# Optimization experiments

Measured on AMD Instinct MI355X. Metric: run time of the kernel, lower is better.

The kernel has to match this reference:

```python
import jax, jax.numpy as jnp
import numpy as np

EPS = 1e-5

def binarize(w):
    # sign() binarization with straight-through estimator (identity grad)
    s = jnp.where(w >= 0, 1.0, -1.0).astype(w.dtype)
    return w + jax.lax.stop_gradient(s - w)

def batchnorm(x, gamma, beta):
    # BatchNorm1d in training mode: biased batch statistics over axis 0
    mean = jnp.mean(x, axis=0)
    var = jnp.mean(jnp.square(x - mean), axis=0)
    return (x - mean) * jax.lax.rsqrt(var + EPS) * gamma + beta

def setup_inputs() -> dict:
    key = jax.random.key(0)
    ks = jax.random.split(key, 3)
    B, D_IN, D_H, D_OUT = 65536, 784, 300, 10
    x = jax.random.normal(ks[0], (B, D_IN), dtype=jnp.float32)
    W1 = jax.random.normal(ks[1], (D_H, D_IN), dtype=jnp.float32) * 0.05
    W2 = jax.random.normal(ks[2], (D_OUT, D_H), dtype=jnp.float32) * 0.05
    gamma1 = jnp.ones((D_H,), jnp.float32)
    beta1 = jnp.zeros((D_H,), jnp.float32)
    gamma2 = jnp.ones((D_OUT,), jnp.float32)
    beta2 = jnp.zeros((D_OUT,), jnp.float32)
    return {"x": x, "W1": W1, "gamma1": gamma1, "beta1": beta1,
            "W2": W2, "gamma2": gamma2, "beta2": beta2}

def reference(x, W1, gamma1, beta1, W2, gamma2, beta2):
    h = x @ binarize(W1).T            # [B, 300]
    h = batchnorm(h, gamma1, beta1)
    o = h @ binarize(W2).T            # [B, 10]
    return batchnorm(o, gamma2, beta2)
```

## Files before the change

kernel.cpp:

```cpp
#include <hip/hip_runtime.h>
#include <cstdint>
#include <cstddef>

#define B_ROWS 65536
#define D_IN   784
#define KP     800
#define D_H    300
#define NP     320
#define D_OUT  10
#define NP2    16
#define EPS    1e-5f
#define NBLK   1024

typedef _Float16 half8  __attribute__((ext_vector_type(8)));
typedef float    floatx4 __attribute__((ext_vector_type(4)));

#define OFF_S1   ((size_t)0)
#define OFF_H    ((size_t)512000)
#define OFF_ZB   (OFF_H + (size_t)41943040)
#define OFF_W2   (OFF_ZB + (size_t)2560)
#define OFF_ST2  (OFF_W2 + (size_t)10240)
#define OFF_OC   (OFF_ST2 + (size_t)256)
#define OFF_P1   OFF_OC
#define OFF_P2   (OFF_OC + (size_t)4194304)

__global__ void k_prep1(const float* __restrict__ W1, _Float16* __restrict__ S1,
                        float* __restrict__ zb)
{
    if (blockIdx.x == 0 && threadIdx.x < 16) zb[threadIdx.x] = 0.0f;
    int idx = blockIdx.x * 256 + threadIdx.x;
    int n = idx / KP;
    int k = idx - n * KP;
    float v = 0.0f;
    if (n < D_H && k < D_IN)
        v = (W1[n * D_IN + k] >= 0.0f) ? 1.0f : -1.0f;
    S1[idx] = (_Float16)v;
}


typedef const __attribute__((address_space(1))) void* gas_p;
typedef __attribute__((address_space(3))) void* las_p;

__device__ __forceinline__ void gload_lds16(const float* g, float* l)
{
    __builtin_amdgcn_global_load_lds((gas_p)g, (las_p)l, 16, 0, 0);
}

#define PF_B(BV, NK)                                                        \
    _Pragma("unroll")                                                       \
    for (int nt = 0; nt < 5; ++nt)                                          \
        BV[nt] = *(const half8*)(bb + (size_t)nt * 16 * KP + (NK));

#define ISSUE_A(BUF, KK)                                                    \
    gload_lds16(gA0 + (KK), &Afl[BUF][0][0] + lof);                         \
    gload_lds16(gA1 + (KK), &Afl[BUF][0][0] + 1024 + lof);

#define ISSUE_A_TAIL(BUF)                                                   \
    gload_lds16(ts0, &Afl[BUF][0][0] + lof);                                \
    gload_lds16(ts1, &Afl[BUF][0][0] + 1024 + lof);

#define AFRAGF(BUF)                                                         \
    _Pragma("unroll")                                                       \
    for (int mt = 0; mt < 4; ++mt) {                                        \
        floatx4 f0 = *(const floatx4*)&Afl[BUF][mt * 16 + row15][ce * 4];   \
        floatx4 f1 = *(const floatx4*)&Afl[BUF][mt * 16 + row15][co * 4];   \
        half8 hv;                                                           \
        _Pragma("unroll")                                                   \
        for (int j = 0; j < 4; ++j) {                                       \
            hv[j]     = (_Float16)f0[j];                                    \
            hv[4 + j] = (_Float16)f1[j];                                    \
        }                                                                   \
        a[mt] = hv;                                                         \
    }

#define COMPUTE(BV)                                                         \
    _Pragma("unroll")                                                       \
    for (int nt = 0; nt < 5; ++nt)                                          \
        _Pragma("unroll")                                                   \
        for (int mt = 0; mt < 4; ++mt)                                      \
            acc[mt][nt] = __builtin_amdgcn_mfma_f32_16x16x32_f16(           \
                a[mt], BV[nt], acc[mt][nt], 0, 0, 0);

#define STEP_SYNC()                                                         \
    __builtin_amdgcn_sched_barrier(0);                                      \
    asm volatile("s_waitcnt vmcnt(5)" ::: "memory");                        \
    __builtin_amdgcn_sched_barrier(0);                                      \
    __builtin_amdgcn_s_barrier();                                           \
    __builtin_amdgcn_sched_barrier(0);

__global__ __launch_bounds__(256) void k_gemm1(const float* __restrict__ x,
                                               const _Float16* __restrict__ S1,
                                               _Float16* __restrict__ h,
                                               float* __restrict__ part,
                                               const float* __restrict__ zb)
{
    __shared__ __align__(16) float Afl[2][64][32];
    const int t     = threadIdx.x;
    const int wave  = t >> 6;
    const int lane  = t & 63;
    const int row15 = lane & 15;
    const int quad  = lane >> 4;
    const int m0    = blockIdx.x * 64;

    const int rA   = wave * 8 + (lane >> 3);
    const int cswz = (lane & 7) ^ ((lane >> 3) & 7);
    const int lof  = wave * 256;
    const float* gA0 = x + (size_t)(m0 + rA) * D_IN + cswz * 4;
    const float* gA1 = gA0 + (size_t)32 * D_IN;
    const float* ts0 = (cswz >= 4) ? zb : (gA0 + 768);
    const float* ts1 = (cswz >= 4) ? zb : (gA1 + 768);

    const int ce = (2 * quad) ^ (row15 & 7);
    const int co = ce ^ 1;

    const _Float16* bb = S1 + (size_t)(wave * 80 + row15) * KP + quad * 8;

    floatx4 acc[4][5] = {};
    half8   b0[5], b1[5];
    half8   a[4];

    ISSUE_A(0, 0)
    __builtin_amdgcn_sched_barrier(0);
    PF_B(b0, 0)
    STEP_SYNC()

    for (int i = 0; i < 12; ++i) {
        const int kk = i * 64;
        ISSUE_A(1, kk + 32)
        __builtin_amdgcn_sched_barrier(0);
        PF_B(b1, kk + 32)
        AFRAGF(0)
        COMPUTE(b0)
        STEP_SYNC()
        if (i < 11) { ISSUE_A(0, kk + 64) } else { ISSUE_A_TAIL(0) }
        __builtin_amdgcn_sched_barrier(0);
        PF_B(b0, kk + 64)
        AFRAGF(1)
        COMPUTE(b1)
        STEP_SYNC()
    }
    AFRAGF(0)
    COMPUTE(b0)

    float s[5] = {}, q[5] = {};
#pragma unroll
    for (int mt = 0; mt < 4; ++mt)
#pragma unroll
        for (int nt = 0; nt < 5; ++nt)
#pragma unroll
            for (int r = 0; r < 4; ++r) {
                float v = acc[mt][nt][r];
                int m = m0 + mt * 16 + quad * 4 + r;
                int n = wave * 80 + nt * 16 + row15;
                h[(size_t)m * NP + n] = (_Float16)v;
                s[nt] += v;
                q[nt] += v * v;
            }
#pragma unroll
    for (int nt = 0; nt < 5; ++nt) {
        s[nt] += __shfl_xor(s[nt], 16); s[nt] += __shfl_xor(s[nt], 32);
        q[nt] += __shfl_xor(q[nt], 16); q[nt] += __shfl_xor(q[nt], 32);
    }
    if (quad == 0) {
#pragma unroll
        for (int nt = 0; nt < 5; ++nt) {
            int col = wave * 80 + nt * 16 + row15;
            part[(size_t)col * NBLK + blockIdx.x]        = s[nt];
            part[(size_t)(NP + col) * NBLK + blockIdx.x] = q[nt];
        }
    }
}

__global__ void k_stat1(const float* __restrict__ part, const float* __restrict__ gamma1,
                        const float* __restrict__ W2, _Float16* __restrict__ w2h)
{
    __shared__ float redS[4], redQ[4];
    const int j = blockIdx.x;
    const int t = threadIdx.x;
    const float* ps = part + (size_t)j * NBLK;
    const float* pq = part + (size_t)(NP + j) * NBLK;
    float s = ps[t] + ps[t + 256] + ps[t + 512] + ps[t + 768];
    float q = pq[t] + pq[t + 256] + pq[t + 512] + pq[t + 768];
#pragma unroll
    for (int off = 1; off < 64; off <<= 1) {
        s += __shfl_xor(s, off);
        q += __shfl_xor(q, off);
    }
    if ((t & 63) == 0) { redS[t >> 6] = s; redQ[t >> 6] = q; }
    __syncthreads();
    if (t < NP2) {
        float S = redS[0] + redS[1] + redS[2] + redS[3];
        float Q = redQ[0] + redQ[1] + redQ[2] + redQ[3];
        float mean = S * (1.0f / 65536.0f);
        float var  = Q * (1.0f / 65536.0f) - mean * mean;
        float a1   = 0.0f;
        if (j < D_H) a1 = gamma1[j] / sqrtf(var + EPS);
        float w = 0.0f;
        if (t < D_OUT && j < D_H)
            w = (W2[t * D_H + j] >= 0.0f) ? a1 : -a1;
        w2h[t * NP + j] = (_Float16)w;
    }
}

__global__ __launch_bounds__(256) void k_gemm2(const _Float16* __restrict__ h,
                                               const _Float16* __restrict__ w2h,
                                               float* __restrict__ oc,
                                               float* __restrict__ part2)
{
    __shared__ _Float16 Wlds[16][328];
    __shared__ float reds[4][16], redq[4][16];
    const int t     = threadIdx.x;
    const int wave  = t >> 6;
    const int lane  = t & 63;
    const int row15 = lane & 15;
    const int quad  = lane >> 4;

    for (int c = t; c < 640; c += 256) {
        int r  = c / 40;
        int cc = (c - r * 40) * 8;
        *(half8*)&Wlds[r][cc] = *(const half8*)(w2h + r * NP + cc);
    }
    __syncthreads();

    const int m0 = blockIdx.x * 64 + wave * 16;
    const _Float16* hp = h + (size_t)(m0 + row15) * NP + quad * 8;
    floatx4 acc = {};
#pragma unroll
    for (int kk = 0; kk < NP; kk += 32) {
        half8 a2 = *(const half8*)(hp + kk);
        half8 b2 = *(const half8*)&Wlds[row15][kk + quad * 8];
        acc = __builtin_amdgcn_mfma_f32_16x16x32_f16(a2, b2, acc, 0, 0, 0);
    }
    float s = 0.f, q = 0.f;
#pragma unroll
    for (int r = 0; r < 4; ++r) {
        float v = acc[r];
        oc[(size_t)(m0 + quad * 4 + r) * NP2 + row15] = v;
        s += v; q += v * v;
    }
    s += __shfl_xor(s, 16); s += __shfl_xor(s, 32);
    q += __shfl_xor(q, 16); q += __shfl_xor(q, 32);
    if (lane < 16) { reds[wave][row15] = s; redq[wave][row15] = q; }
    __syncthreads();
    if (t < 16) {
        float S = reds[0][t] + reds[1][t] + reds[2][t] + reds[3][t];
        float Q = redq[0][t] + redq[1][t] + redq[2][t] + redq[3][t];
        part2[(size_t)t * NBLK + blockIdx.x]          = S;
        part2[(size_t)(16 + t) * NBLK + blockIdx.x]   = Q;
    }
}

__global__ void k_stat2(const float* __restrict__ part2, const float* __restrict__ gamma2,
                        float* __restrict__ st2)
{
    __shared__ float redS[4], redQ[4];
    const int k = blockIdx.x;
    const int t = threadIdx.x;
    const float* ps = part2 + (size_t)k * NBLK;
    const float* pq = part2 + (size_t)(16 + k) * NBLK;
    float s = ps[t] + ps[t + 256] + ps[t + 512] + ps[t + 768];
    float q = pq[t] + pq[t + 256] + pq[t + 512] + pq[t + 768];
#pragma unroll
    for (int off = 1; off < 64; off <<= 1) {
        s += __shfl_xor(s, off);
        q += __shfl_xor(q, off);
    }
    if ((t & 63) == 0) { redS[t >> 6] = s; redQ[t >> 6] = q; }
    __syncthreads();
    if (t == 0) {
        float S = redS[0] + redS[1] + redS[2] + redS[3];
        float Q = redQ[0] + redQ[1] + redQ[2] + redQ[3];
        float mean = S * (1.0f / 65536.0f);
        float var  = Q * (1.0f / 65536.0f) - mean * mean;
        float sc   = (k < D_OUT) ? gamma2[k] / sqrtf(var + EPS) : 0.0f;
        st2[k]      = mean;
        st2[16 + k] = sc;
    }
}

__global__ void k_final(const float* __restrict__ oc, const float* __restrict__ st2,
                        const float* __restrict__ beta2, float* __restrict__ out)
{
    int idx = blockIdx.x * 256 + threadIdx.x;
    int m = idx / 10;
    int k = idx - m * 10;
    float mean = st2[k];
    float sc   = st2[16 + k];
    out[idx] = (oc[(size_t)m * NP2 + k] - mean) * sc + beta2[k];
}

extern "C" void kernel_launch(void* const* d_in, const int* in_sizes, int n_in,
                              void* d_out, int out_size, void* d_ws, size_t ws_size,
                              hipStream_t stream)
{
    const float* x      = (const float*)d_in[0];
    const float* W1     = (const float*)d_in[1];
    const float* gamma1 = (const float*)d_in[2];
    const float* W2     = (const float*)d_in[4];
    const float* gamma2 = (const float*)d_in[5];
    const float* beta2  = (const float*)d_in[6];
    float* out = (float*)d_out;

    char* ws = (char*)d_ws;
    _Float16* S1    = (_Float16*)(ws + OFF_S1);
    _Float16* h     = (_Float16*)(ws + OFF_H);
    float*    zb    = (float*)(ws + OFF_ZB);
    _Float16* w2h   = (_Float16*)(ws + OFF_W2);
    float*    st2   = (float*)(ws + OFF_ST2);
    float*    oc    = (float*)(ws + OFF_OC);
    float*    part  = (float*)(ws + OFF_P1);
    float*    part2 = (float*)(ws + OFF_P2);

    k_prep1 <<<1000, 256, 0, stream>>>(W1, S1, zb);
    k_gemm1 <<<NBLK, 256, 0, stream>>>(x, S1, h, part, zb);
    k_stat1 <<<320, 256, 0, stream>>>(part, gamma1, W2, w2h);
    k_gemm2 <<<NBLK, 256, 0, stream>>>(h, w2h, oc, part2);
    k_stat2 <<<16, 256, 0, stream>>>(part2, gamma2, st2);
    k_final <<<2560, 256, 0, stream>>>(oc, st2, beta2, out);
}
```

Before: 91.79 us.

## Deepen A-tile LDS pipeline in GEMM1 from double to quad buffering

Grows the shared-memory staging buffer for the x tile from two to four slots, so global-to-LDS loads are issued three K-steps ahead instead of one. The main loop is unrolled by four with explicit prologue and epilogue steps, and the vmcnt wait thresholds are adjusted to match the larger number of loads in flight. The aim is to hide more HBM latency behind the MFMA work. In exchange, LDS use per block doubles, which may reduce occupancy, and the hand-tuned wait counts must match the exact issue order.

Measured after the change: 105.3 us. +14.8%, slower.

```diff
diff --git a/kernel.cpp b/kernel.cpp
--- a/kernel.cpp
+++ b/kernel.cpp
@@ -53,11 +53,13 @@
 
 #define ISSUE_A(BUF, KK)                                                    \
     gload_lds16(gA0 + (KK), &Afl[BUF][0][0] + lof);                         \
-    gload_lds16(gA1 + (KK), &Afl[BUF][0][0] + 1024 + lof);
+    gload_lds16(gA1 + (KK), &Afl[BUF][0][0] + 1024 + lof);                  \
+    __builtin_amdgcn_sched_barrier(0);
 
 #define ISSUE_A_TAIL(BUF)                                                   \
     gload_lds16(ts0, &Afl[BUF][0][0] + lof);                                \
-    gload_lds16(ts1, &Afl[BUF][0][0] + 1024 + lof);
+    gload_lds16(ts1, &Afl[BUF][0][0] + 1024 + lof);                         \
+    __builtin_amdgcn_sched_barrier(0);
 
 #define AFRAGF(BUF)                                                         \
     _Pragma("unroll")                                                       \
@@ -81,9 +83,9 @@
             acc[mt][nt] = __builtin_amdgcn_mfma_f32_16x16x32_f16(           \
                 a[mt], BV[nt], acc[mt][nt], 0, 0, 0);
 
-#define STEP_SYNC()                                                         \
+#define STEP_SYNC(N)                                                        \
     __builtin_amdgcn_sched_barrier(0);                                      \
-    asm volatile("s_waitcnt vmcnt(5)" ::: "memory");                        \
+    asm volatile("s_waitcnt vmcnt(" #N ")" ::: "memory");                   \
     __builtin_amdgcn_sched_barrier(0);                                      \
     __builtin_amdgcn_s_barrier();                                           \
     __builtin_amdgcn_sched_barrier(0);
@@ -94,7 +96,7 @@
                                                float* __restrict__ part,
                                                const float* __restrict__ zb)
 {
-    __shared__ __align__(16) float Afl[2][64][32];
+    __shared__ __align__(16) float Afl[4][64][32];
     const int t     = threadIdx.x;
     const int wave  = t >> 6;
     const int lane  = t & 63;
@@ -120,25 +122,52 @@
     half8   a[4];
 
     ISSUE_A(0, 0)
-    __builtin_amdgcn_sched_barrier(0);
+    ISSUE_A(1, 32)
+    ISSUE_A(2, 64)
     PF_B(b0, 0)
-    STEP_SYNC()
-
-    for (int i = 0; i < 12; ++i) {
-        const int kk = i * 64;
-        ISSUE_A(1, kk + 32)
-        __builtin_amdgcn_sched_barrier(0);
+    STEP_SYNC(9)
+
+    for (int i = 0; i < 5; ++i) {
+        const int kk = i * 128;
+        ISSUE_A(3, kk + 96)
         PF_B(b1, kk + 32)
         AFRAGF(0)
         COMPUTE(b0)
-        STEP_SYNC()
-        if (i < 11) { ISSUE_A(0, kk + 64) } else { ISSUE_A_TAIL(0) }
-        __builtin_amdgcn_sched_barrier(0);
+        STEP_SYNC(9)
+        ISSUE_A(0, kk + 128)
         PF_B(b0, kk + 64)
         AFRAGF(1)
         COMPUTE(b1)
-        STEP_SYNC()
-    }
+        STEP_SYNC(9)
+        ISSUE_A(1, kk + 160)
+        PF_B(b1, kk + 96)
+        AFRAGF(2)
+        COMPUTE(b0)
+        STEP_SYNC(9)
+        ISSUE_A(2, kk + 192)
+        PF_B(b0, kk + 128)
+        AFRAGF(3)
+        COMPUTE(b1)
+        STEP_SYNC(9)
+    }
+    ISSUE_A(3, 736)
+    PF_B(b1, 672)
+    AFRAGF(0)
+    COMPUTE(b0)
+    STEP_SYNC(9)
+    ISSUE_A_TAIL(0)
+    PF_B(b0, 704)
+    AFRAGF(1)
+    COMPUTE(b1)
+    STEP_SYNC(9)
+    PF_B(b1, 736)
+    AFRAGF(2)
+    COMPUTE(b0)
+    STEP_SYNC(7)
+    PF_B(b0, 768)
+    AFRAGF(3)
+    COMPUTE(b1)
+    STEP_SYNC(5)
     AFRAGF(0)
     COMPUTE(b0)
 
```
